# Kernel optimization log

Hardware: AMD Instinct MI355X
Metric: run time of the kernel (lower is better)

## Reference

```python
import jax, jax.numpy as jnp
import numpy as np

B, S, D, H = 4, 2048, 768, 12
DEPTH = D // H


def setup_inputs() -> dict:
    key = jax.random.key(0)
    ks = jax.random.split(key, 8)
    scale = 1.0 / np.sqrt(D)
    return {
        "v": jax.random.normal(ks[0], (B, S, D), jnp.float32),
        "k": jax.random.normal(ks[1], (B, S, D), jnp.float32),
        "q": jax.random.normal(ks[2], (B, S, D), jnp.float32),
        "wq": jax.random.normal(ks[3], (D, D), jnp.float32) * scale,
        "wk": jax.random.normal(ks[4], (D, D), jnp.float32) * scale,
        "wv": jax.random.normal(ks[5], (D, D), jnp.float32) * scale,
        "wo": jax.random.normal(ks[6], (D, D), jnp.float32) * scale,
        "bo": jax.random.normal(ks[7], (D,), jnp.float32) * 0.01,
    }


def _split_heads(x):
    # [B, S, D] -> [B, H, S, depth]
    return x.reshape(B, S, H, DEPTH).transpose(0, 2, 1, 3)


def reference(v, k, q, wq, wk, wv, wo, bo):
    # nn.Linear(bias=False): y = x @ W.T
    qh = _split_heads(q @ wq.T)
    kh = _split_heads(k @ wk.T)
    vh = _split_heads(v @ wv.T)
    # scaled dot-product attention (mask=None)
    logits = jnp.einsum("bhqd,bhkd->bhqk", qh, kh) / jnp.sqrt(
        jnp.asarray(DEPTH, jnp.float32)
    )
    attn = jax.nn.softmax(logits, axis=-1)  # [B, H, Sq, Sk]
    out = jnp.einsum("bhqk,bhkd->bhqd", attn, vh)
    concat = out.transpose(0, 2, 1, 3).reshape(B, S, D)
    return concat @ wo.T + bo
```

## Files before the change

### kernel.cpp

```cpp
#include <hip/hip_runtime.h>
#include <math.h>

#define BB 4
#define SS 2048
#define DD 768
#define HH 12
#define DEPTH 64
#define M_TOTAL (BB * SS)
#define WSZ (DD * DD)

typedef __attribute__((ext_vector_type(8))) short bf16x8;
typedef __attribute__((ext_vector_type(16))) float f32x16;
typedef __attribute__((ext_vector_type(4))) float f32x4;
typedef __attribute__((ext_vector_type(4))) unsigned short us4;
typedef __attribute__((ext_vector_type(2))) unsigned int u32x2;

__device__ __forceinline__ unsigned short f2b(float f) {
  unsigned u = __builtin_bit_cast(unsigned, f);
  return (unsigned short)((u + 0x8000u) >> 16);
}

__device__ __forceinline__ unsigned pkrnd(float lo, float hi) {
  unsigned a = __builtin_bit_cast(unsigned, lo) + 0x8000u;
  unsigned b = __builtin_bit_cast(unsigned, hi) + 0x8000u;
  return __builtin_amdgcn_perm(b, a, 0x07060302);
}

__device__ __forceinline__ us4 f2b4(float a, float b, float c, float d) {
  unsigned lo = pkrnd(a, b), hi = pkrnd(c, d);
  us4 t;
  t.x = (unsigned short)lo; t.y = (unsigned short)(lo >> 16);
  t.z = (unsigned short)hi; t.w = (unsigned short)(hi >> 16);
  return t;
}

__device__ __forceinline__ float fexp2(float x) {
  return __builtin_amdgcn_exp2f(x);
}

__device__ __forceinline__ void gl16(const void* g, void* l) {
  __builtin_amdgcn_global_load_lds(
      (const __attribute__((address_space(1))) unsigned int*)g,
      (__attribute__((address_space(3))) unsigned int*)l, 16, 0, 0);
}

__global__ __launch_bounds__(256) void prep(
    const float* __restrict__ s0, const float* __restrict__ s1,
    const float* __restrict__ s2, const float* __restrict__ s3,
    const float* __restrict__ s4, const float* __restrict__ s5,
    const float* __restrict__ s6, unsigned short* __restrict__ d0,
    unsigned short* __restrict__ d1, unsigned short* __restrict__ d2,
    unsigned short* __restrict__ d3, unsigned short* __restrict__ d4,
    unsigned short* __restrict__ d5, unsigned short* __restrict__ d6) {
  const float* s;
  unsigned short* d;
  int n;
  switch (blockIdx.y) {
    case 0: s = s0; d = d0; n = M_TOTAL * DD; break;
    case 1: s = s1; d = d1; n = M_TOTAL * DD; break;
    case 2: s = s2; d = d2; n = M_TOTAL * DD; break;
    case 3: s = s3; d = d3; n = WSZ; break;
    case 4: s = s4; d = d4; n = WSZ; break;
    case 5: s = s5; d = d5; n = WSZ; break;
    default: s = s6; d = d6; n = WSZ; break;
  }
  int idx = (blockIdx.x * 256 + threadIdx.x) * 4;
  if (idx >= n) return;
  float4 f = *(const float4*)(s + idx);
  *(us4*)(d + idx) = f2b4(f.x, f.y, f.z, f.w);
}

__global__ __launch_bounds__(256) void proj_qkv(
    const unsigned short* __restrict__ qb, const unsigned short* __restrict__ kb,
    const unsigned short* __restrict__ vb, const unsigned short* __restrict__ wqb,
    const unsigned short* __restrict__ wkb, const unsigned short* __restrict__ wvb,
    unsigned short* __restrict__ QF, unsigned short* __restrict__ KF,
    unsigned short* __restrict__ VF) {
  const int mode = blockIdx.z;
  const unsigned short* X;
  const unsigned short* W;
  if (mode == 0) { X = qb; W = wqb; }
  else if (mode == 1) { X = kb; W = wkb; }
  else { X = vb; W = wvb; }

  __shared__ __align__(16) char sm[34816];
  unsigned short* As = (unsigned short*)sm;
  unsigned short* Bs = (unsigned short*)(sm + 8192);
  unsigned short* Ts = (unsigned short*)sm;

  const int tid = threadIdx.x;
  const int lane = tid & 63, w_ = tid >> 6;
  const int lr = lane & 15, quad = lane >> 4;
  const int wm = (w_ & 1) * 64, wn = (w_ >> 1) * 64;
  const int m0 = blockIdx.x * 128, n0 = blockIdx.y * 128;
  const int grow = lane >> 2, gcol = (lane & 3) * 8;

  f32x4 acc[4][4];
#pragma unroll
  for (int mt = 0; mt < 4; ++mt)
#pragma unroll
    for (int nt = 0; nt < 4; ++nt) acc[mt][nt] = (f32x4){0.f, 0.f, 0.f, 0.f};

  for (int k0 = 0; k0 < DD; k0 += 32) {
    __syncthreads();
#pragma unroll
    for (int i = 0; i < 2; ++i) {
      int c = 4 * i + w_;
      int row = c * 16 + grow;
      gl16(X + (size_t)(m0 + row) * DD + k0 + gcol, (char*)As + c * 1024);
      gl16(W + (size_t)(n0 + row) * DD + k0 + gcol, (char*)Bs + c * 1024);
    }
    __syncthreads();

    bf16x8 af[4];
#pragma unroll
    for (int mt = 0; mt < 4; ++mt)
      af[mt] = *(const bf16x8*)&As[(wm + 16 * mt + lr) * 32 + 8 * quad];
#pragma unroll
    for (int nt = 0; nt < 4; ++nt) {
      bf16x8 bf = *(const bf16x8*)&Bs[(wn + 16 * nt + lr) * 32 + 8 * quad];
#pragma unroll
      for (int mt = 0; mt < 4; ++mt)
        acc[mt][nt] = __builtin_amdgcn_mfma_f32_16x16x32_bf16(af[mt], bf,
                                                              acc[mt][nt], 0, 0, 0);
    }
  }

  __syncthreads();

  const int b_ = m0 >> 11;
  const int hbase = n0 >> 6;
  const int sgbase = (m0 & 2047) >> 5;

  if (mode < 2) {
    const float osc = (mode == 0) ? 0.18033688011f : 1.0f;
#pragma unroll
    for (int mt = 0; mt < 4; ++mt)
#pragma unroll
      for (int nt = 0; nt < 4; ++nt) {
        int n = wn + 16 * nt + lr;
        int mb = wm + 16 * mt + 4 * quad;
#pragma unroll
        for (int r = 0; r < 4; ++r)
          Ts[(mb + r) * 136 + n] = f2b(acc[mt][nt][r] * osc);
      }
    __syncthreads();
    unsigned short* O = (mode == 0) ? QF : KF;
    const int ks = tid >> 6, lane2 = tid & 63;
    const int mrow = lane2 & 31, hb = lane2 >> 5;
#pragma unroll
    for (int c = 0; c < 8; ++c) {
      int hl = c >> 2, sblk = c & 3;
      int bh = b_ * HH + hbase + hl;
      bf16x8 vv = *(const bf16x8*)&Ts[(sblk * 32 + mrow) * 136 + hl * 64 +
                                      ks * 16 + hb * 8];
      *(bf16x8*)(O + ((size_t)bh * 64 + sgbase + sblk) * 2048 + tid * 8) = vv;
    }
  } else {
#pragma unroll
    for (int mt = 0; mt < 4; ++mt)
#pragma unroll
      for (int nt = 0; nt < 4; ++nt) {
        int n = wn + 16 * nt + lr;
        int mb = wm + 16 * mt + 4 * quad;
        *(us4*)&Ts[n * 136 + mb] =
            f2b4(acc[mt][nt][0], acc[mt][nt][1], acc[mt][nt][2], acc[mt][nt][3]);
      }
    __syncthreads();
    const int ntv = tid >> 7, ks2 = (tid >> 6) & 1, lane2 = tid & 63;
#pragma unroll
    for (int c = 0; c < 8; ++c) {
      int hl = c >> 2, sblk = c & 3;
      int bh = b_ * HH + hbase + hl;
      bf16x8 vv = *(const bf16x8*)&Ts[(hl * 64 + ntv * 32 + (lane2 & 31)) * 136 +
                                      sblk * 32 + ks2 * 16 + (lane2 >> 5) * 8];
      *(bf16x8*)(VF + ((size_t)bh * 64 + sgbase + sblk) * 2048 + tid * 8) = vv;
    }
  }
}

struct KV {
  bf16x8 k[4];
  bf16x8 v[4];
};

__global__ __launch_bounds__(256) void attn(
    const unsigned short* __restrict__ QF, const unsigned short* __restrict__ KF,
    const unsigned short* __restrict__ VF, unsigned short* __restrict__ cc) {
  __shared__ __align__(16) char smem[19200];
  unsigned short (*Ps)[32][40] = (unsigned short (*)[32][40])smem;
  float (*Osh)[64][36] = (float (*)[64][36])smem;
  float (*Ls)[2][32] = (float (*)[2][32])(smem + 18432);
  float (*Linv)[32] = (float (*)[32])(smem + 18944);

  const int tid = threadIdx.x;
  const int lane = tid & 63, w_ = tid >> 6;
  const int wq = w_ & 1, wk = w_ >> 1;
  const int m32 = lane & 31, h = lane >> 5;
  const int q0 = blockIdx.x * 64;
  const int bh = blockIdx.y;
  const size_t perbh = (size_t)SS * DEPTH;

  const unsigned short* qfb = QF + (size_t)bh * perbh;
  const unsigned short* kfb = KF + (size_t)bh * perbh + (size_t)wk * 2048 + lane * 8;
  const unsigned short* vfb = VF + (size_t)bh * perbh + (size_t)wk * 2048 + lane * 8;

  bf16x8 qf[4];
  {
    const unsigned short* p = qfb + (size_t)((q0 >> 5) + wq) * 2048 + lane * 8;
#pragma unroll
    for (int ks = 0; ks < 4; ++ks) qf[ks] = *(const bf16x8*)(p + ks * 512);
  }

  f32x16 o[2];
#pragma unroll
  for (int nt = 0; nt < 2; ++nt)
#pragma unroll
    for (int r = 0; r < 16; ++r) o[nt][r] = 0.f;
  float l_lane = 0.f;

#define LOADKV(tile, dst)                                                    \
  do {                                                                       \
    const unsigned short* kp_ = kfb + (size_t)(tile) * 4096;                 \
    const unsigned short* vp_ = vfb + (size_t)(tile) * 4096;                 \
    _Pragma("unroll") for (int x_ = 0; x_ < 4; ++x_) {                       \
      (dst).k[x_] = *(const bf16x8*)(kp_ + x_ * 512);                        \
      (dst).v[x_] = *(const bf16x8*)(vp_ + x_ * 512);                        \
    }                                                                        \
  } while (0)

#define TILECOMP(kv)                                                         \
  do {                                                                       \
    f32x16 st;                                                               \
    _Pragma("unroll") for (int r_ = 0; r_ < 16; ++r_) st[r_] = 0.f;          \
    _Pragma("unroll") for (int ks_ = 0; ks_ < 4; ++ks_)                      \
        st = __builtin_amdgcn_mfma_f32_32x32x16_bf16((kv).k[ks_], qf[ks_],   \
                                                     st, 0, 0, 0);           \
    _Pragma("unroll") for (int g_ = 0; g_ < 4; ++g_) {                       \
      float e0 = fexp2(st[4 * g_ + 0]), e1 = fexp2(st[4 * g_ + 1]);          \
      float e2 = fexp2(st[4 * g_ + 2]), e3 = fexp2(st[4 * g_ + 3]);          \
      l_lane += (e0 + e1) + (e2 + e3);                                       \
      u32x2 pp;                                                              \
      pp.x = pkrnd(e0, e1);                                                  \
      pp.y = pkrnd(e2, e3);                                                  \
      *(u32x2*)&Ps[w_][m32][8 * g_ + 4 * h] = pp;                            \
    }                                                                        \
    _Pragma("unroll") for (int ks2_ = 0; ks2_ < 2; ++ks2_) {                 \
      bf16x8 pa = *(const bf16x8*)&Ps[w_][m32][16 * ks2_ + 8 * h];           \
      o[0] = __builtin_amdgcn_mfma_f32_32x32x16_bf16(pa, (kv).v[ks2_],       \
                                                     o[0], 0, 0, 0);         \
      o[1] = __builtin_amdgcn_mfma_f32_32x32x16_bf16(pa, (kv).v[2 + ks2_],   \
                                                     o[1], 0, 0, 0);         \
    }                                                                        \
  } while (0)

  KV b0, b1;
  LOADKV(0, b0);
  for (int t = 0; t < 32; t += 2) {
    LOADKV(t + 1, b1);
    TILECOMP(b0);
    if (t + 2 < 32) LOADKV(t + 2, b0);
    TILECOMP(b1);
  }

  l_lane += __shfl_xor(l_lane, 32);
  if (h == 0) Ls[wq][wk][m32] = l_lane;
  __syncthreads();
  if (wk == 1) {
#pragma unroll
    for (int nt = 0; nt < 2; ++nt)
#pragma unroll
      for (int g = 0; g < 4; ++g) {
        float4 t = make_float4(o[nt][4 * g], o[nt][4 * g + 1], o[nt][4 * g + 2],
                               o[nt][4 * g + 3]);
        *(float4*)&Osh[wq][32 * nt + m32][8 * g + 4 * h] = t;
      }
  } else if (tid < 64) {
    int qq = tid & 31, ww = tid >> 5;
    Linv[ww][qq] = 1.f / (Ls[ww][0][qq] + Ls[ww][1][qq]);
  }
  __syncthreads();
  if (wk == 0) {
    const int b_ = bh / HH, h_ = bh % HH;
#pragma unroll
    for (int g = 0; g < 4; ++g) {
      float4 li = *(const float4*)&Linv[wq][8 * g + 4 * h];
      float lia[4] = {li.x, li.y, li.z, li.w};
#pragma unroll
      for (int nt = 0; nt < 2; ++nt) {
        float4 ot = *(const float4*)&Osh[wq][32 * nt + m32][8 * g + 4 * h];
        float oa[4] = {ot.x, ot.y, ot.z, ot.w};
#pragma unroll
        for (int r = 0; r < 4; ++r) {
          int qg = q0 + 32 * wq + 8 * g + 4 * h + r;
          float val = (o[nt][4 * g + r] + oa[r]) * lia[r];
          cc[((size_t)b_ * SS + qg) * DD + h_ * DEPTH + 32 * nt + m32] = f2b(val);
        }
      }
    }
  }
}

__global__ __launch_bounds__(256) void proj_out(
    const unsigned short* __restrict__ cc, const unsigned short* __restrict__ wob,
    const float* __restrict__ bo, float* __restrict__ out) {
  __shared__ __align__(16) unsigned short As[128 * 32];
  __shared__ __align__(16) unsigned short Bs[128 * 32];

  const int tid = threadIdx.x;
  const int lane = tid & 63, w_ = tid >> 6;
  const int lr = lane & 15, quad = lane >> 4;
  const int wm = (w_ & 1) * 64, wn = (w_ >> 1) * 64;
  const int m0 = blockIdx.x * 128, n0 = blockIdx.y * 128;
  const int grow = lane >> 2, gcol = (lane & 3) * 8;

  f32x4 acc[4][4];
#pragma unroll
  for (int mt = 0; mt < 4; ++mt)
#pragma unroll
    for (int nt = 0; nt < 4; ++nt) acc[mt][nt] = (f32x4){0.f, 0.f, 0.f, 0.f};

  for (int k0 = 0; k0 < DD; k0 += 32) {
    __syncthreads();
#pragma unroll
    for (int i = 0; i < 2; ++i) {
      int c = 4 * i + w_;
      int row = c * 16 + grow;
      gl16(cc + (size_t)(m0 + row) * DD + k0 + gcol, (char*)As + c * 1024);
      gl16(wob + (size_t)(n0 + row) * DD + k0 + gcol, (char*)Bs + c * 1024);
    }
    __syncthreads();

    bf16x8 af[4];
#pragma unroll
    for (int mt = 0; mt < 4; ++mt)
      af[mt] = *(const bf16x8*)&As[(wm + 16 * mt + lr) * 32 + 8 * quad];
#pragma unroll
    for (int nt = 0; nt < 4; ++nt) {
      bf16x8 bf = *(const bf16x8*)&Bs[(wn + 16 * nt + lr) * 32 + 8 * quad];
#pragma unroll
      for (int mt = 0; mt < 4; ++mt)
        acc[mt][nt] = __builtin_amdgcn_mfma_f32_16x16x32_bf16(af[mt], bf,
                                                              acc[mt][nt], 0, 0, 0);
    }
  }

#pragma unroll
  for (int mt = 0; mt < 4; ++mt)
#pragma unroll
    for (int nt = 0; nt < 4; ++nt) {
      int n = n0 + wn + 16 * nt + lr;
      float bias = bo[n];
#pragma unroll
      for (int r = 0; r < 4; ++r) {
        int m = m0 + wm + 16 * mt + 4 * quad + r;
        out[(size_t)m * DD + n] = acc[mt][nt][r] + bias;
      }
    }
}

extern "C" void kernel_launch(void* const* d_in, const int* in_sizes, int n_in,
                              void* d_out, int out_size, void* d_ws,
                              size_t ws_size, hipStream_t stream) {
  const float* v = (const float*)d_in[0];
  const float* k = (const float*)d_in[1];
  const float* q = (const float*)d_in[2];
  const float* wq = (const float*)d_in[3];
  const float* wk = (const float*)d_in[4];
  const float* wv = (const float*)d_in[5];
  const float* wo = (const float*)d_in[6];
  const float* bo = (const float*)d_in[7];
  float* out = (float*)d_out;

  const size_t per = (size_t)BB * HH * SS * DEPTH;
  unsigned short* QF = (unsigned short*)d_ws;
  unsigned short* KF = QF + per;
  unsigned short* VF = KF + per;
  unsigned short* cc = VF + per;
  unsigned short* qb = cc + per;
  unsigned short* kb = qb + per;
  unsigned short* vb = kb + per;
  unsigned short* wqb = vb + per;
  unsigned short* wkb = wqb + WSZ;
  unsigned short* wvb = wkb + WSZ;
  unsigned short* wob = wvb + WSZ;

  dim3 g0(M_TOTAL * DD / 1024, 7);
  prep<<<g0, 256, 0, stream>>>(q, k, v, wq, wk, wv, wo, qb, kb, vb, wqb, wkb,
                               wvb, wob);

  dim3 g1(M_TOTAL / 128, DD / 128, 3);
  proj_qkv<<<g1, 256, 0, stream>>>(qb, kb, vb, wqb, wkb, wvb, QF, KF, VF);

  dim3 g2(SS / 64, BB * HH);
  attn<<<g2, 256, 0, stream>>>(QF, KF, VF, cc);

  dim3 g3(M_TOTAL / 128, DD / 128);
  proj_out<<<g3, 256, 0, stream>>>(cc, wob, bo, out);
}
```

Measured before the change: 276.7 us.

## Keep P tile in registers via permlane32 swap instead of LDS round-trip

The attention inner loop no longer writes the exponentiated scores to shared memory and reads them back in the A-operand layout. Instead it packs them to bf16 with the hardware v_cvt_pk_bf16_f32 instruction and rearranges them across the two half-waves with permlane32_swap. It also adds s_setprio around the MFMA blocks, seeds the first QK MFMA from a zero register, and sets launch_bounds to 4 blocks per CU. This removes LDS traffic and the wait on it from the hot loop. The cost is cross-lane shuffles and a change from the previous add-and-shift rounding to the hardware conversion rounding.

```diff
diff --git a/kernel.cpp b/kernel.cpp
--- a/kernel.cpp
+++ b/kernel.cpp
@@ -14,6 +14,7 @@
 typedef __attribute__((ext_vector_type(4))) float f32x4;
 typedef __attribute__((ext_vector_type(4))) unsigned short us4;
 typedef __attribute__((ext_vector_type(2))) unsigned int u32x2;
+typedef __attribute__((ext_vector_type(4))) unsigned int u32x4;
 
 __device__ __forceinline__ unsigned short f2b(float f) {
   unsigned u = __builtin_bit_cast(unsigned, f);
@@ -32,6 +33,20 @@
   t.x = (unsigned short)lo; t.y = (unsigned short)(lo >> 16);
   t.z = (unsigned short)hi; t.w = (unsigned short)(hi >> 16);
   return t;
+}
+
+__device__ __forceinline__ unsigned cvtpk(float a, float b) {
+  unsigned d;
+  asm("v_cvt_pk_bf16_f32 %0, %1, %2" : "=v"(d) : "v"(a), "v"(b));
+  return d;
+}
+
+__device__ __forceinline__ u32x2 permswap(unsigned a, unsigned b) {
+  auto r = __builtin_amdgcn_permlane32_swap(a, b, false, false);
+  u32x2 out;
+  out.x = r[0];
+  out.y = r[1];
+  return out;
 }
 
 __device__ __forceinline__ float fexp2(float x) {
@@ -184,11 +199,10 @@
   bf16x8 v[4];
 };
 
-__global__ __launch_bounds__(256) void attn(
+__global__ __launch_bounds__(256, 4) void attn(
     const unsigned short* __restrict__ QF, const unsigned short* __restrict__ KF,
     const unsigned short* __restrict__ VF, unsigned short* __restrict__ cc) {
   __shared__ __align__(16) char smem[19200];
-  unsigned short (*Ps)[32][40] = (unsigned short (*)[32][40])smem;
   float (*Osh)[64][36] = (float (*)[64][36])smem;
   float (*Ls)[2][32] = (float (*)[2][32])(smem + 18432);
   float (*Linv)[32] = (float (*)[32])(smem + 18944);
@@ -211,6 +225,10 @@
 #pragma unroll
     for (int ks = 0; ks < 4; ++ks) qf[ks] = *(const bf16x8*)(p + ks * 512);
   }
+
+  f32x16 z16;
+#pragma unroll
+  for (int r = 0; r < 16; ++r) z16[r] = 0.f;
 
   f32x16 o[2];
 #pragma unroll
@@ -231,27 +249,41 @@
 
 #define TILECOMP(kv)                                                         \
   do {                                                                       \
-    f32x16 st;                                                               \
-    _Pragma("unroll") for (int r_ = 0; r_ < 16; ++r_) st[r_] = 0.f;          \
-    _Pragma("unroll") for (int ks_ = 0; ks_ < 4; ++ks_)                      \
+    __builtin_amdgcn_s_setprio(1);                                           \
+    f32x16 st = __builtin_amdgcn_mfma_f32_32x32x16_bf16((kv).k[0], qf[0],    \
+                                                        z16, 0, 0, 0);       \
+    _Pragma("unroll") for (int ks_ = 1; ks_ < 4; ++ks_)                      \
         st = __builtin_amdgcn_mfma_f32_32x32x16_bf16((kv).k[ks_], qf[ks_],   \
                                                      st, 0, 0, 0);           \
-    _Pragma("unroll") for (int g_ = 0; g_ < 4; ++g_) {                       \
-      float e0 = fexp2(st[4 * g_ + 0]), e1 = fexp2(st[4 * g_ + 1]);          \
-      float e2 = fexp2(st[4 * g_ + 2]), e3 = fexp2(st[4 * g_ + 3]);          \
-      l_lane += (e0 + e1) + (e2 + e3);                                       \
-      u32x2 pp;                                                              \
-      pp.x = pkrnd(e0, e1);                                                  \
-      pp.y = pkrnd(e2, e3);                                                  \
-      *(u32x2*)&Ps[w_][m32][8 * g_ + 4 * h] = pp;                            \
-    }                                                                        \
-    _Pragma("unroll") for (int ks2_ = 0; ks2_ < 2; ++ks2_) {                 \
-      bf16x8 pa = *(const bf16x8*)&Ps[w_][m32][16 * ks2_ + 8 * h];           \
-      o[0] = __builtin_amdgcn_mfma_f32_32x32x16_bf16(pa, (kv).v[ks2_],       \
-                                                     o[0], 0, 0, 0);         \
-      o[1] = __builtin_amdgcn_mfma_f32_32x32x16_bf16(pa, (kv).v[2 + ks2_],   \
-                                                     o[1], 0, 0, 0);         \
-    }                                                                        \
+    __builtin_amdgcn_s_setprio(0);                                           \
+    float e_[16];                                                            \
+    _Pragma("unroll") for (int r_ = 0; r_ < 16; ++r_) e_[r_] = fexp2(st[r_]);\
+    _Pragma("unroll") for (int g_ = 0; g_ < 4; ++g_)                         \
+        l_lane += (e_[4 * g_ + 0] + e_[4 * g_ + 1]) +                        \
+                  (e_[4 * g_ + 2] + e_[4 * g_ + 3]);                         \
+    unsigned w00 = cvtpk(e_[0], e_[1]), w01 = cvtpk(e_[2], e_[3]);           \
+    unsigned w10 = cvtpk(e_[4], e_[5]), w11 = cvtpk(e_[6], e_[7]);           \
+    unsigned w20 = cvtpk(e_[8], e_[9]), w21 = cvtpk(e_[10], e_[11]);         \
+    unsigned w30 = cvtpk(e_[12], e_[13]), w31 = cvtpk(e_[14], e_[15]);       \
+    u32x2 r0 = permswap(w00, w10);                                           \
+    u32x2 r1 = permswap(w01, w11);                                           \
+    u32x2 r2 = permswap(w20, w30);                                           \
+    u32x2 r3 = permswap(w21, w31);                                           \
+    u32x4 paw0, paw1;                                                        \
+    paw0.x = r0.x; paw0.y = r1.x; paw0.z = r0.y; paw0.w = r1.y;              \
+    paw1.x = r2.x; paw1.y = r3.x; paw1.z = r2.y; paw1.w = r3.y;              \
+    bf16x8 pa0 = __builtin_bit_cast(bf16x8, paw0);                           \
+    bf16x8 pa1 = __builtin_bit_cast(bf16x8, paw1);                           \
+    __builtin_amdgcn_s_setprio(1);                                           \
+    o[0] = __builtin_amdgcn_mfma_f32_32x32x16_bf16(pa0, (kv).v[0], o[0],     \
+                                                   0, 0, 0);                 \
+    o[1] = __builtin_amdgcn_mfma_f32_32x32x16_bf16(pa0, (kv).v[2], o[1],     \
+                                                   0, 0, 0);                 \
+    o[0] = __builtin_amdgcn_mfma_f32_32x32x16_bf16(pa1, (kv).v[1], o[0],     \
+                                                   0, 0, 0);                 \
+    o[1] = __builtin_amdgcn_mfma_f32_32x32x16_bf16(pa1, (kv).v[3], o[1],     \
+                                                   0, 0, 0);                 \
+    __builtin_amdgcn_s_setprio(0);                                           \
   } while (0)
 
   KV b0, b1;
```

New measurement: 404.7 us. 1.46x slower.
